# Performance work log

Measured on AMD Instinct MI355X. Metric: run time of the kernel, lower is better.

Reference implementation:

```python
import jax, jax.numpy as jnp
import numpy as np
from jax import lax

N_SEG = 196
EMB = 768
HID = 512
BN_EPS = 1e-5


def setup_inputs() -> dict:
    key = jax.random.key(0)
    ks = jax.random.split(key, 10)
    f32 = jnp.float32
    return {
        "img": jax.random.normal(ks[0], (8, 3, 224, 224), f32),
        "segments": jax.random.randint(ks[1], (8, 224, 224), 0, N_SEG).astype(jnp.int32),
        "conv1_w": jax.random.normal(ks[2], (64, 3, 7, 7), f32) * 0.05,
        "conv1_b": jnp.zeros((64,), f32),
        "bn1_g": jnp.ones((64,), f32),
        "bn1_b": jnp.zeros((64,), f32),
        "conv2_w": jax.random.normal(ks[3], (EMB, 64, 3, 3), f32) * 0.05,
        "conv2_b": jnp.zeros((EMB,), f32),
        "bn2_g": jnp.ones((EMB,), f32),
        "bn2_b": jnp.zeros((EMB,), f32),
        "pos_embed": jax.random.normal(ks[4], (N_SEG, EMB), f32),
        "W1": jax.random.normal(ks[5], (EMB, HID), f32) * 0.02,
        "b1": jax.random.normal(ks[6], (HID,), f32) * 0.001,
        "W2": jax.random.normal(ks[7], (HID, EMB), f32) * 0.02,
        "b2": jax.random.normal(ks[8], (EMB,), f32) * 0.001,
    }


def _conv(x, w, b, stride, pad):
    y = lax.conv_general_dilated(x, w, (stride, stride), [(pad, pad), (pad, pad)],
                                 dimension_numbers=("NCHW", "OIHW", "NCHW"))
    return y + b[None, :, None, None]


def _bn(x, g, b):
    # training-mode BatchNorm2d: batch stats over (B, H, W), biased variance
    mu = jnp.mean(x, axis=(0, 2, 3), keepdims=True)
    var = jnp.var(x, axis=(0, 2, 3), keepdims=True)
    return (x - mu) * lax.rsqrt(var + BN_EPS) * g[None, :, None, None] + b[None, :, None, None]


def reference(img, segments, conv1_w, conv1_b, bn1_g, bn1_b, conv2_w, conv2_b,
              bn2_g, bn2_b, pos_embed, W1, b1, W2, b2):
    # feature extractor: conv7x7/s2 -> BN -> ReLU -> conv3x3 -> BN -> ReLU
    f = jax.nn.relu(_bn(_conv(img, conv1_w, conv1_b, 2, 3), bn1_g, bn1_b))
    f = jax.nn.relu(_bn(_conv(f, conv2_w, conv2_b, 1, 1), bn2_g, bn2_b))  # [B,C,Hf,Wf]
    B, C, Hf, Wf = f.shape
    N = Hf * Wf

    # nearest-neighbor downsample of segment map to (Hf, Wf):
    # torch 'nearest': src = floor(dst * in/out)
    H, W = segments.shape[1], segments.shape[2]
    hi = (jnp.arange(Hf) * (H / Hf)).astype(jnp.int32)
    wi = (jnp.arange(Wf) * (W / Wf)).astype(jnp.int32)
    seg = jnp.take(jnp.take(segments, hi, axis=1), wi, axis=2)  # [B,Hf,Wf]
    seg_flat = seg.reshape(B * N)

    # NOTE: source does features.view(B, N, C) on an NCHW tensor (no permute);
    # faithfully replicate as a raw row-major reshape.
    feats = f.reshape(B * N, C)

    pos = pos_embed[seg_flat % N_SEG]  # [B*N, C]
    x = feats + pos

    # mask (segments >= 0) is all-true -> MaskedMLP reduces to a dense MLP
    h = jax.nn.gelu(x @ W1 + b1, approximate=False)  # [B*N, HID]
    y = h @ W2 + b2  # [B*N, C]

    gids = jnp.repeat(jnp.arange(B, dtype=jnp.int32), N) * N_SEG + seg_flat
    tokens = jnp.zeros((B * N_SEG, C), dtype=y.dtype).at[gids].set(y)
    return tokens.reshape(B, N_SEG, C)
```

## Files before the change

### kernel.cpp

```cpp
#include <hip/hip_runtime.h>
#include <hip/hip_bf16.h>

typedef __attribute__((ext_vector_type(4))) float f32x4;
typedef __attribute__((ext_vector_type(8))) short s16x8;
typedef __attribute__((ext_vector_type(4))) short s16x4;
typedef unsigned short u16;
typedef unsigned long long u64;

#define NB 8
#define NP 12544
#define PH 114
#define PP 12996
#define PPR 13056
#define QLIM 12768
#define NSEG 196
#define NTOK (NB*NSEG)
#define EMB 768
#define HID 512
#define AROWS 368
#define NBUCK 32

__device__ __forceinline__ u16 f2b(float v) {
  __hip_bfloat16 h = __float2bfloat16(v);
  return __builtin_bit_cast(u16, h);
}
__device__ __forceinline__ float b2f(u16 u) {
  unsigned int x = ((unsigned int)u) << 16;
  return __builtin_bit_cast(float, x);
}
__device__ __forceinline__ u16 f2h(float v) {
  _Float16 h = (_Float16)v;
  return __builtin_bit_cast(u16, h);
}
__device__ __forceinline__ float h2f(u16 u) {
  _Float16 h = __builtin_bit_cast(_Float16, u);
  return (float)h;
}
__device__ __forceinline__ u64 pack4h(f32x4 v) {
  s16x4 p;
#pragma unroll
  for (int e = 0; e < 4; ++e) p[e] = (short)f2h(v[e]);
  return __builtin_bit_cast(u64, p);
}

__device__ __forceinline__ void gl16(const u16* g, u16* l) {
  __builtin_amdgcn_global_load_lds((const __attribute__((address_space(1))) void*)g,
                                   (__attribute__((address_space(3))) void*)l, 16, 0, 0);
}

#define PR_WR1 (147 * 64)
#define PR_WR2 (9 * 768 * 64)
#define PR_W1T (512 * 768)
#define PR_W2T (768 * 512)
__global__ void k_prep(const float* __restrict__ c1w, const float* __restrict__ c2w,
                       const float* __restrict__ W1, const float* __restrict__ W2,
                       float* __restrict__ wr1, u16* __restrict__ wr2,
                       u16* __restrict__ w1t, u16* __restrict__ w2t) {
  int id = blockIdx.x * 256 + threadIdx.x;
  if (id < PR_WR1) {
    int co = id & 63, k = id >> 6;
    int ci = k / 49, r = k % 49, kh = r / 7, kw = r % 7;
    wr1[k * 64 + co] = c1w[((co * 3 + ci) * 7 + kh) * 7 + kw];
    return;
  }
  id -= PR_WR1;
  if (id < PR_WR2) {
    int ci = id & 63, co = (id >> 6) % 768, tap = id / (64 * 768);
    int kh = tap / 3, kw = tap % 3;
    wr2[((size_t)(tap * 768 + co)) * 64 + ci] = f2b(c2w[((co * 64 + ci) * 3 + kh) * 3 + kw]);
    return;
  }
  id -= PR_WR2;
  if (id < PR_W1T) {
    int k = id % 768, n = id / 768;
    w1t[id] = f2b(W1[(size_t)k * 512 + n]);
    return;
  }
  id -= PR_W1T;
  if (id < PR_W2T) {
    int k = id % 512, n = id / 512;
    w2t[id] = f2b(W2[(size_t)k * 768 + n]);
  }
}

__global__ __launch_bounds__(256) void k_conv1(const float* __restrict__ img,
                                               const float* __restrict__ wr1,
                                               u16* __restrict__ c1,
                                               float* __restrict__ sumb,
                                               float* __restrict__ sqb) {
  int owt = blockIdx.x, oh = blockIdx.y, b = blockIdx.z;
  int t = threadIdx.x;
  __shared__ float xs[3 * 7 * 37];
  __shared__ float ls[64], lq[64];
  if (t < 64) { ls[t] = 0.f; lq[t] = 0.f; }
  int iw0 = owt * 32 - 3;
  int ih0 = oh * 2 - 3;
  for (int i = t; i < 3 * 7 * 37; i += 256) {
    int ci = i / (7 * 37), r = i % (7 * 37), kh = r / 37, cc = r % 37;
    int ih = ih0 + kh, iw = iw0 + cc;
    float v = 0.f;
    if ((unsigned)ih < 224u && (unsigned)iw < 224u)
      v = img[((size_t)(b * 3 + ci) * 224 + ih) * 224 + iw];
    xs[i] = v;
  }
  __syncthreads();
  int co = t & 63, g = t >> 6;
  float a0 = 0.f, a1 = 0.f, a2 = 0.f, a3 = 0.f;
  for (int ci = 0; ci < 3; ++ci)
    for (int kh = 0; kh < 7; ++kh) {
      const float* xrow = &xs[(ci * 7 + kh) * 37];
      const float* wrow = &wr1[(ci * 49 + kh * 7) * 64 + co];
#pragma unroll
      for (int kw = 0; kw < 7; ++kw) {
        float wv = wrow[kw * 64];
        int base = g * 8 + kw;
        a0 += xrow[base + 0] * wv;
        a1 += xrow[base + 2] * wv;
        a2 += xrow[base + 4] * wv;
        a3 += xrow[base + 6] * wv;
      }
    }
  size_t p0 = (size_t)b * NP + oh * 112 + owt * 16 + g * 4;
  c1[(p0 + 0) * 64 + co] = f2b(a0);
  c1[(p0 + 1) * 64 + co] = f2b(a1);
  c1[(p0 + 2) * 64 + co] = f2b(a2);
  c1[(p0 + 3) * 64 + co] = f2b(a3);
  float s = a0 + a1 + a2 + a3;
  float q = a0 * a0 + a1 * a1 + a2 * a2 + a3 * a3;
  atomicAdd(&ls[co], s);
  atomicAdd(&lq[co], q);
  __syncthreads();
  if (t < 64) {
    int bid = owt + 7 * (oh + 112 * b);
    int bk = (bid & (NBUCK - 1)) * 64 + t;
    atomicAdd(&sumb[bk], ls[t]);
    atomicAdd(&sqb[bk], lq[t]);
  }
}

__global__ void k_bncoef(const float* __restrict__ sumb, const float* __restrict__ sqb,
                         const float* __restrict__ g, const float* __restrict__ bb,
                         float* __restrict__ a, float* __restrict__ s, int C, float invN,
                         int nbuck) {
  int i = blockIdx.x * 256 + threadIdx.x;
  if (i >= C) return;
  float ms = 0.f, qs = 0.f;
  for (int k = 0; k < nbuck; ++k) { ms += sumb[k * C + i]; qs += sqb[k * C + i]; }
  float m = ms * invN;
  float v = qs * invN - m * m;
  float ai = g[i] * rsqrtf(v + 1e-5f);
  a[i] = ai;
  s[i] = bb[i] - m * ai;
}

__global__ __launch_bounds__(256) void k_norm_xp(const u16* __restrict__ c1,
                                                 const float* __restrict__ a1,
                                                 const float* __restrict__ s1,
                                                 u16* __restrict__ xp) {
  int id = blockIdx.x * 256 + threadIdx.x;
  if (id >= NB * NP * 8) return;
  int pix = id >> 3;
  int c8 = (id & 7) * 8;
  int b = pix / NP, p = pix % NP;
  s16x8 v = *(const s16x8*)&c1[(size_t)pix * 64 + c8];
  s16x8 o;
#pragma unroll
  for (int e = 0; e < 8; ++e) {
    float val = b2f((u16)v[e]);
    float r = fmaxf(a1[c8 + e] * val + s1[c8 + e], 0.f);
    o[e] = (short)f2b(r);
  }
  int oh = p / 112, ow = p % 112;
  *(s16x8*)&xp[((size_t)b * PP + (size_t)(oh + 1) * PH + (ow + 1)) * 64 + c8] = o;
}

__global__ __launch_bounds__(256, 2) void k_conv2_stats(const u16* __restrict__ xp,
                                                        const u16* __restrict__ wr2,
                                                        float* __restrict__ sum,
                                                        float* __restrict__ sq,
                                                        u16* __restrict__ y) {
  const int t = threadIdx.x;
  const int lane = t & 63;
  const int w = t >> 6;
  const int wr = w >> 1, wc = w & 1;
  const int h = blockIdx.x;
  const int b = h & 7;
  const int r8 = h >> 3;
  const int q0 = (r8 / 6) * 128;
  const int co0 = (r8 % 6) * 128;
  const int la = lane & 15, lb = lane >> 4;

  __shared__ __align__(16) u16 As[AROWS * 64];
  __shared__ __align__(16) u16 Bs[2][128 * 64];
  __shared__ float csum[128], csq[128];
  if (t < 128) { csum[t] = 0.f; csq[t] = 0.f; }

  const size_t xbase = (size_t)b * PP;

#define BSTAGE(tap, buf) do {                                                   \
    const u16* bsrc_ = wr2 + ((size_t)((tap) * 768 + co0)) * 64;                 \
    _Pragma("unroll")                                                            \
    for (int i_ = 0; i_ < 4; ++i_) {                                             \
      int s_ = i_ * 256 + w * 64 + lane;                                         \
      int r_ = s_ >> 3, c_ = s_ & 7;                                             \
      int cg_ = c_ ^ (r_ & 7);                                                   \
      gl16(bsrc_ + (size_t)r_ * 64 + cg_ * 8,                                    \
           &Bs[buf][(size_t)(i_ * 256 + w * 64) * 8]);                           \
    }                                                                            \
  } while (0)

  BSTAGE(0, 0);
  {
    const u16* src = xp + (xbase + q0) * 64;
#pragma unroll
    for (int i = 0; i < 12; ++i) {
      int s = i * 256 + t;
      if (s < AROWS * 8) {
        int r = s >> 3, c = s & 7;
        int cg = c ^ (r & 7);
        f32x4 v = *(const f32x4*)(src + (size_t)r * 64 + cg * 8);
        *(f32x4*)&As[(size_t)s * 8] = v;
      }
    }
  }
  __syncthreads();

  const f32x4 zero4 = {0.f, 0.f, 0.f, 0.f};
  f32x4 acc[4][4];
#pragma unroll
  for (int i = 0; i < 4; ++i)
#pragma unroll
    for (int j = 0; j < 4; ++j) acc[i][j] = zero4;

  for (int tap = 0; tap < 9; ++tap) {
    const int off = (tap / 3) * PH + (tap % 3);
    const int buf = tap & 1;

    s16x8 af[4][2], bf[4][2];
#pragma unroll
    for (int qf = 0; qf < 4; ++qf) {
      int r = wr * 64 + qf * 16 + la + off;
      int rx = r & 7;
#pragma unroll
      for (int ks = 0; ks < 2; ++ks) {
        int slot = (ks * 4 + lb) ^ rx;
        af[qf][ks] = *(const s16x8*)&As[r * 64 + slot * 8];
      }
    }
#pragma unroll
    for (int cf = 0; cf < 4; ++cf) {
      int r = wc * 64 + cf * 16 + la;
      int rx = r & 7;
#pragma unroll
      for (int ks = 0; ks < 2; ++ks) {
        int slot = (ks * 4 + lb) ^ rx;
        bf[cf][ks] = *(const s16x8*)&Bs[buf][r * 64 + slot * 8];
      }
    }

    if (tap < 8) BSTAGE(tap + 1, buf ^ 1);

#pragma unroll
    for (int ks = 0; ks < 2; ++ks)
#pragma unroll
      for (int qf = 0; qf < 4; ++qf)
#pragma unroll
        for (int cf = 0; cf < 4; ++cf)
          acc[qf][cf] = __builtin_amdgcn_mfma_f32_16x16x32_bf16(af[qf][ks], bf[cf][ks], acc[qf][cf], 0, 0, 0);

    __syncthreads();
  }
#undef BSTAGE

  u64* S = (u64*)As;
#pragma unroll
  for (int cf = 0; cf < 4; ++cf) {
    int row = wc * 64 + cf * 16 + la;
#pragma unroll
    for (int qf = 0; qf < 4; ++qf) {
      int chunk = wr * 16 + qf * 4 + lb;
      S[row * 32 + (chunk ^ (row & 15))] = pack4h(acc[qf][cf]);
    }
  }

  bool vmask[16];
#pragma unroll
  for (int qf = 0; qf < 4; ++qf)
#pragma unroll
    for (int rr = 0; rr < 4; ++rr) {
      int q = q0 + wr * 64 + qf * 16 + lb * 4 + rr;
      vmask[qf * 4 + rr] = (q < QLIM) && ((q % PH) < 112);
    }
#pragma unroll
  for (int cf = 0; cf < 4; ++cf) {
    const int cob = wc * 64 + cf * 16 + la;
    float s = 0.f, ss = 0.f;
#pragma unroll
    for (int qf = 0; qf < 4; ++qf)
#pragma unroll
      for (int rr = 0; rr < 4; ++rr) {
        float v = acc[qf][cf][rr];
        if (vmask[qf * 4 + rr]) { s += v; ss += v * v; }
      }
    s += __shfl_xor(s, 16); ss += __shfl_xor(ss, 16);
    s += __shfl_xor(s, 32); ss += __shfl_xor(ss, 32);
    if (lane < 16) { atomicAdd(&csum[cob], s); atomicAdd(&csq[cob], ss); }
  }
  __syncthreads();

  {
    const size_t ybb = ((size_t)b * EMB + co0) * PPR + q0;
#pragma unroll
    for (int i = 0; i < 16; ++i) {
      int g = i * 256 + t;
      int row = g >> 5, c = g & 31;
      u64 pk = S[row * 32 + (c ^ (row & 15))];
      *(u64*)&y[ybb + (size_t)row * PPR + c * 4] = pk;
    }
  }
  if (t < 128) { atomicAdd(&sum[co0 + t], csum[t]); atomicAdd(&sq[co0 + t], csq[t]); }
}

__global__ void k_lastn(const int* __restrict__ seg, int* __restrict__ lastn) {
  int id = blockIdx.x * 256 + threadIdx.x;
  if (id >= NB * NP) return;
  int b = id / NP, n = id % NP;
  int oh = n / 112, ow = n % 112;
  int s = seg[((size_t)b * 224 + oh * 2) * 224 + ow * 2];
  if ((unsigned)s < 196u) atomicMax(&lastn[b * NSEG + s], n);
}

__global__ __launch_bounds__(256) void k_token_out(const u16* __restrict__ y,
                                                   const int* __restrict__ lastn,
                                                   const float* __restrict__ a2,
                                                   const float* __restrict__ s2,
                                                   const float* __restrict__ pos,
                                                   u16* __restrict__ x) {
  int tok = blockIdx.x;
  int b = tok / NSEG, sg = tok % NSEG;
  int n = lastn[tok];
  int t = threadIdx.x;
  for (int c = t; c < EMB; c += 256) {
    float r = 0.f;
    if (n >= 0) {
      int j = n * EMB + c;
      int ch = j / NP, sp = j - ch * NP;
      int qd = sp / 112, qm = sp - qd * 112;
      float v = h2f(y[((size_t)b * EMB + ch) * PPR + qd * PH + qm]);
      r = fmaxf(a2[ch] * v + s2[ch], 0.f) + pos[(size_t)sg * EMB + c];
    }
    x[(size_t)tok * EMB + c] = f2b(r);
  }
}

__global__ __launch_bounds__(256) void k_mlp1(const u16* __restrict__ x,
                                              const u16* __restrict__ w1t,
                                              const float* __restrict__ b1,
                                              u16* __restrict__ h) {
  int t = threadIdx.x, lane = t & 63, w = t >> 6;
  int la = lane & 15, lb = lane >> 4;
  int m0 = (blockIdx.x * 4 + w) * 16;
  int n0 = blockIdx.y * 64;
  const f32x4 zero4 = {0.f, 0.f, 0.f, 0.f};
  f32x4 acc[4] = {zero4, zero4, zero4, zero4};
  int mrow = m0 + la; if (mrow >= NTOK) mrow = NTOK - 1;
  for (int k = 0; k < EMB; k += 32) {
    int ko = k + lb * 8;
    s16x8 a = *(const s16x8*)(x + (size_t)mrow * EMB + ko);
#pragma unroll
    for (int cf = 0; cf < 4; ++cf) {
      s16x8 bv = *(const s16x8*)(w1t + (size_t)(n0 + cf * 16 + la) * EMB + ko);
      acc[cf] = __builtin_amdgcn_mfma_f32_16x16x32_bf16(a, bv, acc[cf], 0, 0, 0);
    }
  }
#pragma unroll
  for (int cf = 0; cf < 4; ++cf) {
    int n = n0 + cf * 16 + la;
    float bias = b1[n];
#pragma unroll
    for (int r = 0; r < 4; ++r) {
      int m = m0 + lb * 4 + r;
      if (m < NTOK) {
        float v = acc[cf][r] + bias;
        float gg = 0.5f * v * (1.f + erff(v * 0.70710678118654752f));
        h[(size_t)m * HID + n] = f2b(gg);
      }
    }
  }
}

__global__ __launch_bounds__(256) void k_mlp2(const u16* __restrict__ h,
                                              const u16* __restrict__ w2t,
                                              const float* __restrict__ b2,
                                              const int* __restrict__ lastn,
                                              float* __restrict__ out) {
  int t = threadIdx.x, lane = t & 63, w = t >> 6;
  int la = lane & 15, lb = lane >> 4;
  int m0 = (blockIdx.x * 4 + w) * 16;
  int n0 = blockIdx.y * 64;
  const f32x4 zero4 = {0.f, 0.f, 0.f, 0.f};
  f32x4 acc[4] = {zero4, zero4, zero4, zero4};
  int mrow = m0 + la; if (mrow >= NTOK) mrow = NTOK - 1;
  for (int k = 0; k < HID; k += 32) {
    int ko = k + lb * 8;
    s16x8 a = *(const s16x8*)(h + (size_t)mrow * HID + ko);
#pragma unroll
    for (int cf = 0; cf < 4; ++cf) {
      s16x8 bv = *(const s16x8*)(w2t + (size_t)(n0 + cf * 16 + la) * HID + ko);
      acc[cf] = __builtin_amdgcn_mfma_f32_16x16x32_bf16(a, bv, acc[cf], 0, 0, 0);
    }
  }
#pragma unroll
  for (int cf = 0; cf < 4; ++cf) {
    int n = n0 + cf * 16 + la;
    float bias = b2[n];
#pragma unroll
    for (int r = 0; r < 4; ++r) {
      int m = m0 + lb * 4 + r;
      if (m < NTOK && lastn[m] >= 0)
        out[(size_t)m * EMB + n] = acc[cf][r] + bias;
    }
  }
}

extern "C" void kernel_launch(void* const* d_in, const int* in_sizes, int n_in,
                              void* d_out, int out_size, void* d_ws, size_t ws_size,
                              hipStream_t stream) {
  const float* img  = (const float*)d_in[0];
  const int*   seg  = (const int*)  d_in[1];
  const float* c1w  = (const float*)d_in[2];
  const float* bn1g = (const float*)d_in[4];
  const float* bn1b = (const float*)d_in[5];
  const float* c2w  = (const float*)d_in[6];
  const float* bn2g = (const float*)d_in[8];
  const float* bn2b = (const float*)d_in[9];
  const float* pos  = (const float*)d_in[10];
  const float* W1   = (const float*)d_in[11];
  const float* b1   = (const float*)d_in[12];
  const float* W2   = (const float*)d_in[13];
  const float* b2   = (const float*)d_in[14];

  char* ws = (char*)d_ws;
  size_t off = 0;
  auto alloc = [&](size_t bytes) { size_t o = off; off = (off + bytes + 255) & ~(size_t)255; return o; };

  const size_t xpRows = (size_t)NB * PP + 512;
  size_t oXp  = alloc(xpRows * 64 * 2);
  size_t oC1  = alloc((size_t)NB * NP * 64 * 2);
  size_t oY   = alloc((size_t)NB * EMB * PPR * 2);
  size_t oWr2 = alloc((size_t)9 * 768 * 64 * 2);
  size_t oWr1 = alloc(147 * 64 * 4);
  size_t oW1T = alloc((size_t)HID * EMB * 2);
  size_t oW2T = alloc((size_t)EMB * HID * 2);
  size_t oSum = alloc((NBUCK * 64 * 2 + 768 + 768) * 4);
  size_t oCoef = alloc((64 + 64 + 768 + 768) * 4);
  size_t oLast = alloc(NTOK * 4);
  size_t oX   = alloc((size_t)NTOK * EMB * 2);
  size_t oH   = alloc((size_t)NTOK * HID * 2);
  (void)ws_size; (void)in_sizes; (void)n_in;

  u16*   xp   = (u16*)(ws + oXp);
  u16*   c1   = (u16*)(ws + oC1);
  u16*   y    = (u16*)(ws + oY);
  u16*   wr2  = (u16*)(ws + oWr2);
  float* wr1  = (float*)(ws + oWr1);
  u16*   w1t  = (u16*)(ws + oW1T);
  u16*   w2t  = (u16*)(ws + oW2T);
  float* bn1sumb = (float*)(ws + oSum);
  float* bn1sqb  = bn1sumb + NBUCK * 64;
  float* bn2sum  = bn1sumb + NBUCK * 64 * 2;
  float* bn2sq   = bn2sum + 768;
  float* a1 = (float*)(ws + oCoef);
  float* s1 = a1 + 64;
  float* a2 = a1 + 128;
  float* s2 = a2 + 768;
  int*   lastn = (int*)(ws + oLast);
  u16*   x  = (u16*)(ws + oX);
  u16*   h  = (u16*)(ws + oH);
  float* out = (float*)d_out;

  hipMemsetAsync(ws + oXp, 0, xpRows * 64 * 2, stream);
  hipMemsetAsync(ws + oSum, 0, (NBUCK * 64 * 2 + 768 + 768) * 4, stream);
  hipMemsetAsync(ws + oLast, 0xFF, NTOK * 4, stream);
  hipMemsetAsync(d_out, 0, (size_t)out_size * 4, stream);

  const int prep_total = PR_WR1 + PR_WR2 + PR_W1T + PR_W2T;
  k_prep<<<(prep_total + 255) / 256, 256, 0, stream>>>(c1w, c2w, W1, W2, wr1, wr2, w1t, w2t);
  k_lastn<<<392, 256, 0, stream>>>(seg, lastn);

  k_conv1<<<dim3(7, 112, 8), 256, 0, stream>>>(img, wr1, c1, bn1sumb, bn1sqb);
  k_bncoef<<<1, 256, 0, stream>>>(bn1sumb, bn1sqb, bn1g, bn1b, a1, s1, 64, 1.f / 100352.f, NBUCK);
  k_norm_xp<<<(NB * NP * 8) / 256, 256, 0, stream>>>(c1, a1, s1, xp);

  k_conv2_stats<<<4800, 256, 0, stream>>>(xp, wr2, bn2sum, bn2sq, y);
  k_bncoef<<<3, 256, 0, stream>>>(bn2sum, bn2sq, bn2g, bn2b, a2, s2, 768, 1.f / 100352.f, 1);

  k_token_out<<<NTOK, 256, 0, stream>>>(y, lastn, a2, s2, pos, x);

  k_mlp1<<<dim3(25, 8), 256, 0, stream>>>(x, w1t, b1, h);
  k_mlp2<<<dim3(25, 12), 256, 0, stream>>>(h, w2t, b2, lastn, out);
}
```

Before: 264.1 us.

## Load conv2 activation fragments directly from global memory, drop LDS A tile

The conv2 implicit-GEMM kernel no longer stages the 368-row activation halo tile in shared memory. Each wave now reads its A fragments for every tap straight from global memory (relying on cache for reuse across the 9 taps). The per-tap fragment loads are split by k-step so fewer registers stay live. With the LDS footprint reduced, launch bounds are raised to 4 blocks per CU. This trades LDS capacity and staging cost for repeated uncoalesced global/L2 loads in the inner loop, which may expose latency.

```diff
diff --git a/kernel.cpp b/kernel.cpp
--- a/kernel.cpp
+++ b/kernel.cpp
@@ -17,7 +17,6 @@
 #define NTOK (NB*NSEG)
 #define EMB 768
 #define HID 512
-#define AROWS 368
 #define NBUCK 32
 
 __device__ __forceinline__ u16 f2b(float v) {
@@ -174,7 +173,7 @@
   *(s16x8*)&xp[((size_t)b * PP + (size_t)(oh + 1) * PH + (ow + 1)) * 64 + c8] = o;
 }
 
-__global__ __launch_bounds__(256, 2) void k_conv2_stats(const u16* __restrict__ xp,
+__global__ __launch_bounds__(256, 4) void k_conv2_stats(const u16* __restrict__ xp,
                                                         const u16* __restrict__ wr2,
                                                         float* __restrict__ sum,
                                                         float* __restrict__ sq,
@@ -190,8 +189,7 @@
   const int co0 = (r8 % 6) * 128;
   const int la = lane & 15, lb = lane >> 4;
 
-  __shared__ __align__(16) u16 As[AROWS * 64];
-  __shared__ __align__(16) u16 Bs[2][128 * 64];
+  __shared__ __align__(16) u16 Bs[2][8192];
   __shared__ float csum[128], csq[128];
   if (t < 128) { csum[t] = 0.f; csq[t] = 0.f; }
 
@@ -210,19 +208,6 @@
   } while (0)
 
   BSTAGE(0, 0);
-  {
-    const u16* src = xp + (xbase + q0) * 64;
-#pragma unroll
-    for (int i = 0; i < 12; ++i) {
-      int s = i * 256 + t;
-      if (s < AROWS * 8) {
-        int r = s >> 3, c = s & 7;
-        int cg = c ^ (r & 7);
-        f32x4 v = *(const f32x4*)(src + (size_t)r * 64 + cg * 8);
-        *(f32x4*)&As[(size_t)s * 8] = v;
-      }
-    }
-  }
   __syncthreads();
 
   const f32x4 zero4 = {0.f, 0.f, 0.f, 0.f};
@@ -231,48 +216,38 @@
   for (int i = 0; i < 4; ++i)
 #pragma unroll
     for (int j = 0; j < 4; ++j) acc[i][j] = zero4;
+
+  const u16* arow = xp + (xbase + (size_t)(q0 + wr * 64 + la)) * 64 + lb * 8;
 
   for (int tap = 0; tap < 9; ++tap) {
     const int off = (tap / 3) * PH + (tap % 3);
     const int buf = tap & 1;
 
-    s16x8 af[4][2], bf[4][2];
-#pragma unroll
-    for (int qf = 0; qf < 4; ++qf) {
-      int r = wr * 64 + qf * 16 + la + off;
-      int rx = r & 7;
-#pragma unroll
-      for (int ks = 0; ks < 2; ++ks) {
-        int slot = (ks * 4 + lb) ^ rx;
-        af[qf][ks] = *(const s16x8*)&As[r * 64 + slot * 8];
+#pragma unroll
+    for (int ks = 0; ks < 2; ++ks) {
+      s16x8 af[4], bf[4];
+#pragma unroll
+      for (int qf = 0; qf < 4; ++qf)
+        af[qf] = *(const s16x8*)(arow + (size_t)(qf * 16 + off) * 64 + ks * 32);
+#pragma unroll
+      for (int cf = 0; cf < 4; ++cf) {
+        int r = wc * 64 + cf * 16 + la;
+        int slot = (ks * 4 + lb) ^ (r & 7);
+        bf[cf] = *(const s16x8*)&Bs[buf][r * 64 + slot * 8];
       }
-    }
-#pragma unroll
-    for (int cf = 0; cf < 4; ++cf) {
-      int r = wc * 64 + cf * 16 + la;
-      int rx = r & 7;
-#pragma unroll
-      for (int ks = 0; ks < 2; ++ks) {
-        int slot = (ks * 4 + lb) ^ rx;
-        bf[cf][ks] = *(const s16x8*)&Bs[buf][r * 64 + slot * 8];
-      }
-    }
-
-    if (tap < 8) BSTAGE(tap + 1, buf ^ 1);
-
-#pragma unroll
-    for (int ks = 0; ks < 2; ++ks)
+      if (ks == 0 && tap < 8) BSTAGE(tap + 1, buf ^ 1);
 #pragma unroll
       for (int qf = 0; qf < 4; ++qf)
 #pragma unroll
         for (int cf = 0; cf < 4; ++cf)
-          acc[qf][cf] = __builtin_amdgcn_mfma_f32_16x16x32_bf16(af[qf][ks], bf[cf][ks], acc[qf][cf], 0, 0, 0);
+          acc[qf][cf] = __builtin_amdgcn_mfma_f32_16x16x32_bf16(af[qf], bf[cf], acc[qf][cf], 0, 0, 0);
+    }
 
     __syncthreads();
   }
 #undef BSTAGE
 
-  u64* S = (u64*)As;
+  u64* S = (u64*)Bs;
 #pragma unroll
   for (int cf = 0; cf < 4; ++cf) {
     int row = wc * 64 + cf * 16 + la;
```

After: 353.2 us. 1.34x slower.

## Gather only surviving token rows directly from conv2 tile instead of full output

Applied to the files above, without the earlier changes.

The conv2 epilogue no longer writes the full pre-BN conv2 output (8x768x13056 fp16) to global memory. A pixel-to-token map built from the last-writer indices lets each block write only the raw conv2 values that land in surviving token rows, straight from shared memory into a compact token buffer. The token kernel then reads that compact buffer. This removes roughly 160 MB of global writes, at the cost of a scalar, divergent scatter loop in the epilogue plus an extra small kernel and a memset for the map.

```diff
diff --git a/kernel.cpp b/kernel.cpp
--- a/kernel.cpp
+++ b/kernel.cpp
@@ -11,7 +11,6 @@
 #define NP 12544
 #define PH 114
 #define PP 12996
-#define PPR 13056
 #define QLIM 12768
 #define NSEG 196
 #define NTOK (NB*NSEG)
@@ -174,11 +173,28 @@
   *(s16x8*)&xp[((size_t)b * PP + (size_t)(oh + 1) * PH + (ow + 1)) * 64 + c8] = o;
 }
 
+__global__ void k_lastn(const int* __restrict__ seg, int* __restrict__ lastn) {
+  int id = blockIdx.x * 256 + threadIdx.x;
+  if (id >= NB * NP) return;
+  int b = id / NP, n = id % NP;
+  int oh = n / 112, ow = n % 112;
+  int s = seg[((size_t)b * 224 + oh * 2) * 224 + ow * 2];
+  if ((unsigned)s < 196u) atomicMax(&lastn[b * NSEG + s], n);
+}
+
+__global__ void k_tokmap(const int* __restrict__ lastn, int* __restrict__ tokn) {
+  int tok = blockIdx.x * 256 + threadIdx.x;
+  if (tok >= NTOK) return;
+  int n = lastn[tok];
+  if (n >= 0) tokn[(tok / NSEG) * NP + n] = tok;
+}
+
 __global__ __launch_bounds__(256, 2) void k_conv2_stats(const u16* __restrict__ xp,
                                                         const u16* __restrict__ wr2,
+                                                        const int* __restrict__ tokn,
                                                         float* __restrict__ sum,
                                                         float* __restrict__ sq,
-                                                        u16* __restrict__ y) {
+                                                        u16* __restrict__ xr) {
   const int t = threadIdx.x;
   const int lane = t & 63;
   const int w = t >> 6;
@@ -309,44 +325,50 @@
   __syncthreads();
 
   {
-    const size_t ybb = ((size_t)b * EMB + co0) * PPR + q0;
-#pragma unroll
-    for (int i = 0; i < 16; ++i) {
-      int g = i * 256 + t;
-      int row = g >> 5, c = g & 31;
-      u64 pk = S[row * 32 + (c ^ (row & 15))];
-      *(u64*)&y[ybb + (size_t)row * PPR + c * 4] = pk;
+    int qd0 = q0 / PH, qm0 = q0 % PH;
+    int s0 = qd0 * 112 + (qm0 < 112 ? qm0 : 112);
+    int qe = q0 + 127; if (qe >= QLIM) qe = QLIM - 1;
+    int qd1 = qe / PH, qm1 = qe % PH;
+    int s1 = qd1 * 112 + (qm1 < 112 ? qm1 : 111);
+    const u16* Su = (const u16*)As;
+    int ci = t & 127, nsel = t >> 7;
+    int co = co0 + ci;
+    int jlo = co * NP + s0, jhi = co * NP + s1;
+    int n = jlo / 768 + nsel;
+    if (n <= jhi / 768) {
+      int tok = tokn[b * NP + n];
+      if (tok >= 0) {
+        int ja = n * 768, jb = ja + 767;
+        if (ja < jlo) ja = jlo;
+        if (jb > jhi) jb = jhi;
+        for (int j = ja; j <= jb; ++j) {
+          int c = j - n * 768;
+          int sp = j - co * NP;
+          int qloc = (sp / 112) * PH + (sp % 112) - q0;
+          u16 v = Su[(ci * 32 + ((qloc >> 2) ^ (ci & 15))) * 4 + (qloc & 3)];
+          xr[(size_t)tok * EMB + c] = v;
+        }
+      }
     }
   }
   if (t < 128) { atomicAdd(&sum[co0 + t], csum[t]); atomicAdd(&sq[co0 + t], csq[t]); }
 }
 
-__global__ void k_lastn(const int* __restrict__ seg, int* __restrict__ lastn) {
-  int id = blockIdx.x * 256 + threadIdx.x;
-  if (id >= NB * NP) return;
-  int b = id / NP, n = id % NP;
-  int oh = n / 112, ow = n % 112;
-  int s = seg[((size_t)b * 224 + oh * 2) * 224 + ow * 2];
-  if ((unsigned)s < 196u) atomicMax(&lastn[b * NSEG + s], n);
-}
-
-__global__ __launch_bounds__(256) void k_token_out(const u16* __restrict__ y,
+__global__ __launch_bounds__(256) void k_token_out(const u16* __restrict__ xr,
                                                    const int* __restrict__ lastn,
                                                    const float* __restrict__ a2,
                                                    const float* __restrict__ s2,
                                                    const float* __restrict__ pos,
                                                    u16* __restrict__ x) {
   int tok = blockIdx.x;
-  int b = tok / NSEG, sg = tok % NSEG;
+  int sg = tok % NSEG;
   int n = lastn[tok];
   int t = threadIdx.x;
   for (int c = t; c < EMB; c += 256) {
     float r = 0.f;
     if (n >= 0) {
-      int j = n * EMB + c;
-      int ch = j / NP, sp = j - ch * NP;
-      int qd = sp / 112, qm = sp - qd * 112;
-      float v = h2f(y[((size_t)b * EMB + ch) * PPR + qd * PH + qm]);
+      int ch = (n * EMB + c) / NP;
+      float v = h2f(xr[(size_t)tok * EMB + c]);
       r = fmaxf(a2[ch] * v + s2[ch], 0.f) + pos[(size_t)sg * EMB + c];
     }
     x[(size_t)tok * EMB + c] = f2b(r);
@@ -447,7 +469,7 @@
   const size_t xpRows = (size_t)NB * PP + 512;
   size_t oXp  = alloc(xpRows * 64 * 2);
   size_t oC1  = alloc((size_t)NB * NP * 64 * 2);
-  size_t oY   = alloc((size_t)NB * EMB * PPR * 2);
+  size_t oXr  = alloc((size_t)NTOK * EMB * 2);
   size_t oWr2 = alloc((size_t)9 * 768 * 64 * 2);
   size_t oWr1 = alloc(147 * 64 * 4);
   size_t oW1T = alloc((size_t)HID * EMB * 2);
@@ -455,13 +477,14 @@
   size_t oSum = alloc((NBUCK * 64 * 2 + 768 + 768) * 4);
   size_t oCoef = alloc((64 + 64 + 768 + 768) * 4);
   size_t oLast = alloc(NTOK * 4);
+  size_t oTokn = alloc((size_t)NB * NP * 4);
   size_t oX   = alloc((size_t)NTOK * EMB * 2);
   size_t oH   = alloc((size_t)NTOK * HID * 2);
   (void)ws_size; (void)in_sizes; (void)n_in;
 
   u16*   xp   = (u16*)(ws + oXp);
   u16*   c1   = (u16*)(ws + oC1);
-  u16*   y    = (u16*)(ws + oY);
+  u16*   xr   = (u16*)(ws + oXr);
   u16*   wr2  = (u16*)(ws + oWr2);
   float* wr1  = (float*)(ws + oWr1);
   u16*   w1t  = (u16*)(ws + oW1T);
@@ -475,6 +498,7 @@
   float* a2 = a1 + 128;
   float* s2 = a2 + 768;
   int*   lastn = (int*)(ws + oLast);
+  int*   tokn  = (int*)(ws + oTokn);
   u16*   x  = (u16*)(ws + oX);
   u16*   h  = (u16*)(ws + oH);
   float* out = (float*)d_out;
@@ -482,20 +506,22 @@
   hipMemsetAsync(ws + oXp, 0, xpRows * 64 * 2, stream);
   hipMemsetAsync(ws + oSum, 0, (NBUCK * 64 * 2 + 768 + 768) * 4, stream);
   hipMemsetAsync(ws + oLast, 0xFF, NTOK * 4, stream);
+  hipMemsetAsync(ws + oTokn, 0xFF, (size_t)NB * NP * 4, stream);
   hipMemsetAsync(d_out, 0, (size_t)out_size * 4, stream);
 
   const int prep_total = PR_WR1 + PR_WR2 + PR_W1T + PR_W2T;
   k_prep<<<(prep_total + 255) / 256, 256, 0, stream>>>(c1w, c2w, W1, W2, wr1, wr2, w1t, w2t);
   k_lastn<<<392, 256, 0, stream>>>(seg, lastn);
+  k_tokmap<<<(NTOK + 255) / 256, 256, 0, stream>>>(lastn, tokn);
 
   k_conv1<<<dim3(7, 112, 8), 256, 0, stream>>>(img, wr1, c1, bn1sumb, bn1sqb);
   k_bncoef<<<1, 256, 0, stream>>>(bn1sumb, bn1sqb, bn1g, bn1b, a1, s1, 64, 1.f / 100352.f, NBUCK);
   k_norm_xp<<<(NB * NP * 8) / 256, 256, 0, stream>>>(c1, a1, s1, xp);
 
-  k_conv2_stats<<<4800, 256, 0, stream>>>(xp, wr2, bn2sum, bn2sq, y);
+  k_conv2_stats<<<4800, 256, 0, stream>>>(xp, wr2, tokn, bn2sum, bn2sq, xr);
   k_bncoef<<<3, 256, 0, stream>>>(bn2sum, bn2sq, bn2g, bn2b, a2, s2, 768, 1.f / 100352.f, 1);
 
-  k_token_out<<<NTOK, 256, 0, stream>>>(y, lastn, a2, s2, pos, x);
+  k_token_out<<<NTOK, 256, 0, stream>>>(xr, lastn, a2, s2, pos, x);
 
   k_mlp1<<<dim3(25, 8), 256, 0, stream>>>(x, w1t, b1, h);
   k_mlp2<<<dim3(25, 12), 256, 0, stream>>>(h, w2t, b2, lastn, out);
```

After: 280.0 us. 6.0% more time.

## Fuse BN1+ReLU into conv2 tile load, merge lastn into prep, drop memsets

Applied to the files above, without the earlier changes.

Removes the separate normalize-and-pad kernel and its zero-filled padded buffer. conv2 now reads raw conv1 output, applies BN1 scale/shift and ReLU while staging its A tile into LDS, and writes zeros for out-of-bounds padding. The lastn scatter is folded into the prep kernel, and the output memset is replaced by mlp2 writing zeros for empty token slots. This saves a full write and read of the padded activation plus several launches and memsets. In exchange, each conv2 block repeats the normalization for its overlapping halo rows, and the per-element index math and conditionals are added to the LDS staging loop.

```diff
diff --git a/kernel.cpp b/kernel.cpp
--- a/kernel.cpp
+++ b/kernel.cpp
@@ -52,10 +52,13 @@
 #define PR_WR2 (9 * 768 * 64)
 #define PR_W1T (512 * 768)
 #define PR_W2T (768 * 512)
+#define PR_LASTN (NB * NP)
 __global__ void k_prep(const float* __restrict__ c1w, const float* __restrict__ c2w,
                        const float* __restrict__ W1, const float* __restrict__ W2,
+                       const int* __restrict__ seg,
                        float* __restrict__ wr1, u16* __restrict__ wr2,
-                       u16* __restrict__ w1t, u16* __restrict__ w2t) {
+                       u16* __restrict__ w1t, u16* __restrict__ w2t,
+                       int* __restrict__ lastn) {
   int id = blockIdx.x * 256 + threadIdx.x;
   if (id < PR_WR1) {
     int co = id & 63, k = id >> 6;
@@ -80,6 +83,14 @@
   if (id < PR_W2T) {
     int k = id % 512, n = id / 512;
     w2t[id] = f2b(W2[(size_t)k * 768 + n]);
+    return;
+  }
+  id -= PR_W2T;
+  if (id < PR_LASTN) {
+    int b = id / NP, n = id % NP;
+    int oh = n / 112, ow = n % 112;
+    int s = seg[((size_t)b * 224 + oh * 2) * 224 + ow * 2];
+    if ((unsigned)s < 196u) atomicMax(&lastn[b * NSEG + s], n);
   }
 }
 
@@ -153,29 +164,10 @@
   s[i] = bb[i] - m * ai;
 }
 
-__global__ __launch_bounds__(256) void k_norm_xp(const u16* __restrict__ c1,
-                                                 const float* __restrict__ a1,
-                                                 const float* __restrict__ s1,
-                                                 u16* __restrict__ xp) {
-  int id = blockIdx.x * 256 + threadIdx.x;
-  if (id >= NB * NP * 8) return;
-  int pix = id >> 3;
-  int c8 = (id & 7) * 8;
-  int b = pix / NP, p = pix % NP;
-  s16x8 v = *(const s16x8*)&c1[(size_t)pix * 64 + c8];
-  s16x8 o;
-#pragma unroll
-  for (int e = 0; e < 8; ++e) {
-    float val = b2f((u16)v[e]);
-    float r = fmaxf(a1[c8 + e] * val + s1[c8 + e], 0.f);
-    o[e] = (short)f2b(r);
-  }
-  int oh = p / 112, ow = p % 112;
-  *(s16x8*)&xp[((size_t)b * PP + (size_t)(oh + 1) * PH + (ow + 1)) * 64 + c8] = o;
-}
-
-__global__ __launch_bounds__(256, 2) void k_conv2_stats(const u16* __restrict__ xp,
+__global__ __launch_bounds__(256, 2) void k_conv2_stats(const u16* __restrict__ c1,
                                                         const u16* __restrict__ wr2,
+                                                        const float* __restrict__ a1,
+                                                        const float* __restrict__ s1,
                                                         float* __restrict__ sum,
                                                         float* __restrict__ sq,
                                                         u16* __restrict__ y) {
@@ -195,8 +187,6 @@
   __shared__ float csum[128], csq[128];
   if (t < 128) { csum[t] = 0.f; csq[t] = 0.f; }
 
-  const size_t xbase = (size_t)b * PP;
-
 #define BSTAGE(tap, buf) do {                                                   \
     const u16* bsrc_ = wr2 + ((size_t)((tap) * 768 + co0)) * 64;                 \
     _Pragma("unroll")                                                            \
@@ -211,15 +201,30 @@
 
   BSTAGE(0, 0);
   {
-    const u16* src = xp + (xbase + q0) * 64;
+    const u16* c1b = c1 + (size_t)b * NP * 64;
+    const int c = t & 7;
+    f32x4 aLo = *(const f32x4*)&a1[c * 8];
+    f32x4 aHi = *(const f32x4*)&a1[c * 8 + 4];
+    f32x4 sLo = *(const f32x4*)&s1[c * 8];
+    f32x4 sHi = *(const f32x4*)&s1[c * 8 + 4];
 #pragma unroll
     for (int i = 0; i < 12; ++i) {
       int s = i * 256 + t;
       if (s < AROWS * 8) {
-        int r = s >> 3, c = s & 7;
-        int cg = c ^ (r & 7);
-        f32x4 v = *(const f32x4*)(src + (size_t)r * 64 + cg * 8);
-        *(f32x4*)&As[(size_t)s * 8] = v;
+        int r = s >> 3;
+        int p = q0 + r;
+        int pd = p / PH, pm = p - pd * PH;
+        s16x8 o = {0, 0, 0, 0, 0, 0, 0, 0};
+        if (pd >= 1 && pd <= 112 && pm >= 1 && pm <= 112) {
+          int pix = (pd - 1) * 112 + (pm - 1);
+          s16x8 v = *(const s16x8*)&c1b[(size_t)pix * 64 + c * 8];
+#pragma unroll
+          for (int e = 0; e < 4; ++e) {
+            o[e]     = (short)f2b(fmaxf(aLo[e] * b2f((u16)v[e])     + sLo[e], 0.f));
+            o[e + 4] = (short)f2b(fmaxf(aHi[e] * b2f((u16)v[e + 4]) + sHi[e], 0.f));
+          }
+        }
+        *(s16x8*)&As[r * 64 + ((c ^ (r & 7)) * 8)] = o;
       }
     }
   }
@@ -319,15 +324,6 @@
     }
   }
   if (t < 128) { atomicAdd(&sum[co0 + t], csum[t]); atomicAdd(&sq[co0 + t], csq[t]); }
-}
-
-__global__ void k_lastn(const int* __restrict__ seg, int* __restrict__ lastn) {
-  int id = blockIdx.x * 256 + threadIdx.x;
-  if (id >= NB * NP) return;
-  int b = id / NP, n = id % NP;
-  int oh = n / 112, ow = n % 112;
-  int s = seg[((size_t)b * 224 + oh * 2) * 224 + ow * 2];
-  if ((unsigned)s < 196u) atomicMax(&lastn[b * NSEG + s], n);
 }
 
 __global__ __launch_bounds__(256) void k_token_out(const u16* __restrict__ y,
@@ -417,8 +413,8 @@
 #pragma unroll
     for (int r = 0; r < 4; ++r) {
       int m = m0 + lb * 4 + r;
-      if (m < NTOK && lastn[m] >= 0)
-        out[(size_t)m * EMB + n] = acc[cf][r] + bias;
+      if (m < NTOK)
+        out[(size_t)m * EMB + n] = (lastn[m] >= 0) ? (acc[cf][r] + bias) : 0.f;
     }
   }
 }
@@ -444,8 +440,6 @@
   size_t off = 0;
   auto alloc = [&](size_t bytes) { size_t o = off; off = (off + bytes + 255) & ~(size_t)255; return o; };
 
-  const size_t xpRows = (size_t)NB * PP + 512;
-  size_t oXp  = alloc(xpRows * 64 * 2);
   size_t oC1  = alloc((size_t)NB * NP * 64 * 2);
   size_t oY   = alloc((size_t)NB * EMB * PPR * 2);
   size_t oWr2 = alloc((size_t)9 * 768 * 64 * 2);
@@ -459,7 +453,6 @@
   size_t oH   = alloc((size_t)NTOK * HID * 2);
   (void)ws_size; (void)in_sizes; (void)n_in;
 
-  u16*   xp   = (u16*)(ws + oXp);
   u16*   c1   = (u16*)(ws + oC1);
   u16*   y    = (u16*)(ws + oY);
   u16*   wr2  = (u16*)(ws + oWr2);
@@ -479,20 +472,17 @@
   u16*   h  = (u16*)(ws + oH);
   float* out = (float*)d_out;
 
-  hipMemsetAsync(ws + oXp, 0, xpRows * 64 * 2, stream);
   hipMemsetAsync(ws + oSum, 0, (NBUCK * 64 * 2 + 768 + 768) * 4, stream);
   hipMemsetAsync(ws + oLast, 0xFF, NTOK * 4, stream);
-  hipMemsetAsync(d_out, 0, (size_t)out_size * 4, stream);
-
-  const int prep_total = PR_WR1 + PR_WR2 + PR_W1T + PR_W2T;
-  k_prep<<<(prep_total + 255) / 256, 256, 0, stream>>>(c1w, c2w, W1, W2, wr1, wr2, w1t, w2t);
-  k_lastn<<<392, 256, 0, stream>>>(seg, lastn);
+
+  const int prep_total = PR_WR1 + PR_WR2 + PR_W1T + PR_W2T + PR_LASTN;
+  k_prep<<<(prep_total + 255) / 256, 256, 0, stream>>>(c1w, c2w, W1, W2, seg,
+                                                        wr1, wr2, w1t, w2t, lastn);
 
   k_conv1<<<dim3(7, 112, 8), 256, 0, stream>>>(img, wr1, c1, bn1sumb, bn1sqb);
   k_bncoef<<<1, 256, 0, stream>>>(bn1sumb, bn1sqb, bn1g, bn1b, a1, s1, 64, 1.f / 100352.f, NBUCK);
-  k_norm_xp<<<(NB * NP * 8) / 256, 256, 0, stream>>>(c1, a1, s1, xp);
-
-  k_conv2_stats<<<4800, 256, 0, stream>>>(xp, wr2, bn2sum, bn2sq, y);
+
+  k_conv2_stats<<<4800, 256, 0, stream>>>(c1, wr2, a1, s1, bn2sum, bn2sq, y);
   k_bncoef<<<3, 256, 0, stream>>>(bn2sum, bn2sq, bn2g, bn2b, a2, s2, 768, 1.f / 100352.f, 1);
 
   k_token_out<<<NTOK, 256, 0, stream>>>(y, lastn, a2, s2, pos, x);
```

New measurement: 268.6 us. Within noise of the previous version (+1.7%).
